# Performance work log

Measured on AMD Instinct MI355X. Metric: run time of the kernel, lower is better.

Reference implementation:

```python
import jax, jax.numpy as jnp
import numpy as np

EPS = 1e-12  # matches torch F.normalize eps


def setup_inputs() -> dict:
    key = jax.random.key(0)
    k1, k2, k3 = jax.random.split(key, 3)
    N, C, H, W, K = 16, 1024, 32, 32, 32
    x = jax.random.normal(k1, (N, C, H, W), dtype=jnp.float32)
    # 1x1 conv weight (K, C, 1, 1) stored as (K, C)
    conv_w = jax.random.normal(k2, (K, C), dtype=jnp.float32) * 0.02
    centroids = jax.random.uniform(k3, (K, C), dtype=jnp.float32)
    return {"x": x, "conv_w": conv_w, "centroids": centroids}


def _l2norm(v, axis):
    return v / jnp.maximum(jnp.linalg.norm(v, axis=axis, keepdims=True), EPS)


def reference(x, conv_w, centroids):
    N, C, H, W = x.shape
    K = centroids.shape[0]
    # normalize_input: L2 over channel dim
    x = _l2norm(x, axis=1)
    xf = x.reshape(N, C, H * W)                      # (N, C, P)
    # 1x1 conv == per-pixel matmul -> (N, K, P)
    logits = jnp.einsum('kc,ncp->nkp', conv_w, xf)
    a = jax.nn.softmax(logits, axis=1)               # softmax over clusters
    # sum_p a[n,k,p] * (x[n,:,p] - centroids[k,:])
    # == (a @ x^T) - (sum_p a) * centroids  (two GEMMs, no (N,K,C,P) blowup)
    vlad = jnp.einsum('nkp,ncp->nkc', a, xf) - a.sum(-1)[:, :, None] * centroids[None]
    vlad = _l2norm(vlad, axis=2)                     # intra-cluster L2 norm
    vlad = vlad.reshape(N, K * C)
    vlad = _l2norm(vlad, axis=1)                     # global L2 norm
    return vlad
```

## Files before the change

### kernel.cpp

```cpp
#include <hip/hip_runtime.h>

#define NB   16
#define CC   1024
#define PP   1024
#define KK   32
#define EPSF 1e-12f

typedef __attribute__((ext_vector_type(8))) short  bf16x8;
typedef __attribute__((ext_vector_type(4))) float  f32x4;

__device__ __forceinline__ float bf2f(unsigned short u) {
    union { unsigned int i; float f; } v; v.i = ((unsigned int)u) << 16; return v.f;
}
__device__ __forceinline__ unsigned short f2bf(float f) {
    union { float f; unsigned int i; } v; v.f = f;
    return (unsigned short)((v.i + 0x7fffu + ((v.i >> 16) & 1u)) >> 16);
}

template <typename T> struct IO;
template <> struct IO<float> {
    static __device__ __forceinline__ float  ld (const float* p) { return *p; }
    static __device__ __forceinline__ float4 ld4(const float* p) { return *(const float4*)p; }
};
template <> struct IO<unsigned short> {
    static __device__ __forceinline__ float  ld (const unsigned short* p) { return bf2f(*p); }
    static __device__ __forceinline__ float4 ld4(const unsigned short* p) {
        const ushort4 u = *(const ushort4*)p;
        return make_float4(bf2f(u.x), bf2f(u.y), bf2f(u.z), bf2f(u.w));
    }
};

__global__ __launch_bounds__(256) void k_detect(const unsigned short* __restrict__ xu,
                                                int* __restrict__ flag) {
    __shared__ int s;
    const int t = threadIdx.x;
    if (t == 0) s = 0;
    __syncthreads();
    int bad = 0;
    for (int i = t; i < 4096; i += 256)
        if (((xu[i] >> 7) & 0xFFu) > 0x9Fu) bad = 1;
    if (bad) atomicOr(&s, 1);
    __syncthreads();
    if (t == 0) flag[0] = s;
}

template <typename T>
__device__ __forceinline__ void attn_body(const T* __restrict__ x,
                                          const T* __restrict__ w,
                                          float* __restrict__ rnorm_ws,
                                          unsigned short* __restrict__ attn_g,
                                          float* __restrict__ asum) {
    __shared__ __align__(16) unsigned short xt[32 * 136];
    __shared__ __align__(16) unsigned short w_lds[32 * 136];
    __shared__ float red[32 * 32];
    __shared__ float lg[32 * 33];
    __shared__ float inv_lds[32];
    __shared__ float rnorm_lds[32];
    const int b = blockIdx.x, t = threadIdx.x;
    const int n = b >> 5, pbase = (b & 31) * 32;
    const int lane = t & 63, wv = t >> 6;
    const int quad = lane >> 4, l15 = lane & 15;
    const int mt = wv & 1, nt = wv >> 1;

    const size_t xb = (size_t)n * CC * PP + pbase;
    float ss0 = 0.f, ss1 = 0.f, ss2 = 0.f, ss3 = 0.f;
    f32x4 acc = {0.f, 0.f, 0.f, 0.f};

    const int pxg = 4 * (t & 7);
    const int crow = t >> 3;

    for (int ch = 0; ch < 8; ++ch) {
        const int c0 = ch * 128;
        __syncthreads();
        #pragma unroll
        for (int pass = 0; pass < 4; ++pass) {
            const int cl = crow + 32 * pass;
            const float4 v = IO<T>::ld4(&x[xb + (size_t)(c0 + cl) * PP + pxg]);
            ss0 += v.x * v.x; ss1 += v.y * v.y; ss2 += v.z * v.z; ss3 += v.w * v.w;
            xt[(pxg + 0) * 136 + cl] = f2bf(v.x);
            xt[(pxg + 1) * 136 + cl] = f2bf(v.y);
            xt[(pxg + 2) * 136 + cl] = f2bf(v.z);
            xt[(pxg + 3) * 136 + cl] = f2bf(v.w);
        }
        {
            const int k = t >> 3, cg = (t & 7) * 16;
            #pragma unroll
            for (int j = 0; j < 4; ++j) {
                const float4 v = IO<T>::ld4(&w[k * CC + c0 + cg + 4 * j]);
                ushort4 u;
                u.x = f2bf(v.x); u.y = f2bf(v.y); u.z = f2bf(v.z); u.w = f2bf(v.w);
                *(ushort4*)&w_lds[k * 136 + cg + 4 * j] = u;
            }
        }
        __syncthreads();
        #pragma unroll
        for (int ks = 0; ks < 4; ++ks) {
            const bf16x8 av = *(const bf16x8*)&xt[(mt * 16 + l15) * 136 + ks * 32 + quad * 8];
            const bf16x8 bv = *(const bf16x8*)&w_lds[(nt * 16 + l15) * 136 + ks * 32 + quad * 8];
            acc = __builtin_amdgcn_mfma_f32_16x16x32_bf16(av, bv, acc, 0, 0, 0);
        }
    }
    red[crow * 32 + pxg + 0] = ss0;
    red[crow * 32 + pxg + 1] = ss1;
    red[crow * 32 + pxg + 2] = ss2;
    red[crow * 32 + pxg + 3] = ss3;
    __syncthreads();
    if (t < 32) {
        float s = 0.f;
        #pragma unroll
        for (int g = 0; g < 32; ++g) s += red[g * 32 + t];
        const float r = 1.0f / fmaxf(sqrtf(s), EPSF);
        rnorm_lds[t] = r;
        rnorm_ws[n * PP + pbase + t] = r;
    }
    __syncthreads();
    #pragma unroll
    for (int reg = 0; reg < 4; ++reg) {
        const int px = mt * 16 + quad * 4 + reg;
        lg[px * 33 + nt * 16 + l15] = acc[reg] * rnorm_lds[px];
    }
    __syncthreads();
    if (t < 32) {
        float m = -1e30f;
        #pragma unroll
        for (int k = 0; k < KK; ++k) m = fmaxf(m, lg[t * 33 + k]);
        float s = 0.f;
        #pragma unroll
        for (int k = 0; k < KK; ++k) {
            const float e = expf(lg[t * 33 + k] - m);
            lg[t * 33 + k] = e;
            s += e;
        }
        inv_lds[t] = 1.0f / s;
    }
    __syncthreads();
    {
        const int k = t >> 3;
        float s = 0.f;
        ushort4 u;
        float vv[4];
        #pragma unroll
        for (int j = 0; j < 4; ++j) {
            const int px = pxg + j;
            vv[j] = lg[px * 33 + k] * inv_lds[px];
        }
        u.x = f2bf(vv[0]); u.y = f2bf(vv[1]); u.z = f2bf(vv[2]); u.w = f2bf(vv[3]);
        s = bf2f(u.x) + bf2f(u.y) + bf2f(u.z) + bf2f(u.w);
        *(ushort4*)&attn_g[((size_t)n * KK + k) * PP + pbase + pxg] = u;
        s += __shfl_xor(s, 1, 64);
        s += __shfl_xor(s, 2, 64);
        s += __shfl_xor(s, 4, 64);
        if ((t & 7) == 0) atomicAdd(&asum[n * KK + k], s);
    }
}
__global__ __launch_bounds__(256) void k_attn(const void* __restrict__ x,
                                              const void* __restrict__ w,
                                              const int* __restrict__ flag,
                                              float* __restrict__ rnorm_ws,
                                              unsigned short* __restrict__ attn_g,
                                              float* __restrict__ asum) {
    if (*flag) attn_body<float>((const float*)x, (const float*)w, rnorm_ws, attn_g, asum);
    else       attn_body<unsigned short>((const unsigned short*)x, (const unsigned short*)w,
                                         rnorm_ws, attn_g, asum);
}

template <typename T>
__device__ __forceinline__ void vlad_body(const T* __restrict__ x,
                                          const T* __restrict__ cent,
                                          const float* __restrict__ rnorm_ws,
                                          const unsigned short* __restrict__ attn_g,
                                          const float* __restrict__ asum,
                                          float* __restrict__ vlad,
                                          float* __restrict__ ssqnk) {
    __shared__ __align__(16) unsigned short xt[64 * 136];
    __shared__ __align__(16) unsigned short at_lds[32 * 136];
    __shared__ float asum_lds[32];
    __shared__ float ssq_lds[32];
    const int b = blockIdx.x, t = threadIdx.x;
    const int n = b >> 4, cbase = (b & 15) * 64;
    const int lane = t & 63, wv = t >> 6;
    const int quad = lane >> 4, l15 = lane & 15;
    const int mt = wv & 1, nt0 = (wv >> 1) * 2, nt1 = nt0 + 1;

    if (t < 32) { asum_lds[t] = asum[n * KK + t]; ssq_lds[t] = 0.f; }

    f32x4 acc0 = {0.f, 0.f, 0.f, 0.f}, acc1 = {0.f, 0.f, 0.f, 0.f};
    const size_t xb = (size_t)n * CC * PP + (size_t)cbase * PP;

    for (int pc = 0; pc < 8; ++pc) {
        const int p0 = pc * 128;
        __syncthreads();
        {
            const int k = t >> 3, pg = (t & 7) * 16;
            const size_t base = ((size_t)n * KK + k) * PP + p0 + pg;
            const uint4 u0 = *(const uint4*)&attn_g[base];
            const uint4 u1 = *(const uint4*)&attn_g[base + 8];
            *(uint4*)&at_lds[k * 136 + pg]     = u0;
            *(uint4*)&at_lds[k * 136 + pg + 8] = u1;
        }
        {
            const int pg = 4 * (t & 31);
            const float4 rn = *(const float4*)&rnorm_ws[n * PP + p0 + pg];
            #pragma unroll
            for (int pass = 0; pass < 8; ++pass) {
                const int ci = (t >> 5) + 8 * pass;
                const float4 v = IO<T>::ld4(&x[xb + (size_t)ci * PP + p0 + pg]);
                ushort4 u;
                u.x = f2bf(v.x * rn.x); u.y = f2bf(v.y * rn.y);
                u.z = f2bf(v.z * rn.z); u.w = f2bf(v.w * rn.w);
                *(ushort4*)&xt[ci * 136 + pg] = u;
            }
        }
        __syncthreads();
        #pragma unroll
        for (int ks = 0; ks < 4; ++ks) {
            const bf16x8 av  = *(const bf16x8*)&at_lds[(mt * 16 + l15) * 136 + ks * 32 + quad * 8];
            const bf16x8 bv0 = *(const bf16x8*)&xt[(nt0 * 16 + l15) * 136 + ks * 32 + quad * 8];
            const bf16x8 bv1 = *(const bf16x8*)&xt[(nt1 * 16 + l15) * 136 + ks * 32 + quad * 8];
            acc0 = __builtin_amdgcn_mfma_f32_16x16x32_bf16(av, bv0, acc0, 0, 0, 0);
            acc1 = __builtin_amdgcn_mfma_f32_16x16x32_bf16(av, bv1, acc1, 0, 0, 0);
        }
    }
    __syncthreads();
    const int c0g = cbase + nt0 * 16 + l15, c1g = cbase + nt1 * 16 + l15;
    #pragma unroll
    for (int reg = 0; reg < 4; ++reg) {
        const int k = mt * 16 + quad * 4 + reg;
        const float A = asum_lds[k];
        const float v0 = acc0[reg] - A * IO<T>::ld(&cent[k * CC + c0g]);
        const float v1 = acc1[reg] - A * IO<T>::ld(&cent[k * CC + c1g]);
        vlad[((size_t)n * KK + k) * CC + c0g] = v0;
        vlad[((size_t)n * KK + k) * CC + c1g] = v1;
        float s = v0 * v0 + v1 * v1;
        s += __shfl_xor(s, 1, 64);
        s += __shfl_xor(s, 2, 64);
        s += __shfl_xor(s, 4, 64);
        s += __shfl_xor(s, 8, 64);
        if (l15 == 0) atomicAdd(&ssq_lds[k], s);
    }
    __syncthreads();
    if (t < 32) atomicAdd(&ssqnk[n * KK + t], ssq_lds[t]);
}
__global__ __launch_bounds__(256) void k_vlad(const void* __restrict__ x,
                                              const void* __restrict__ cent,
                                              const int* __restrict__ flag,
                                              const float* __restrict__ rnorm_ws,
                                              const unsigned short* __restrict__ attn_g,
                                              const float* __restrict__ asum,
                                              float* __restrict__ vlad,
                                              float* __restrict__ ssqnk) {
    if (*flag) vlad_body<float>((const float*)x, (const float*)cent, rnorm_ws, attn_g,
                                asum, vlad, ssqnk);
    else       vlad_body<unsigned short>((const unsigned short*)x, (const unsigned short*)cent,
                                         rnorm_ws, attn_g, asum, vlad, ssqnk);
}

__global__ __launch_bounds__(64) void k_factors(const float* __restrict__ ssqnk,
                                                float* __restrict__ rintra,
                                                float* __restrict__ rglob) {
    const int n = blockIdx.x, t = threadIdx.x;
    const float s = (t < KK) ? ssqnk[n * KK + t] : 0.f;
    const float r = 1.0f / fmaxf(sqrtf(s), EPSF);
    if (t < KK) rintra[n * KK + t] = r;
    float g = s * r * r;
    for (int off = 32; off > 0; off >>= 1) g += __shfl_down(g, off, 64);
    if (t == 0) rglob[n] = 1.0f / fmaxf(sqrtf(g), EPSF);
}

__global__ __launch_bounds__(256) void k_out(const float* __restrict__ vlad,
                                             const float* __restrict__ rintra,
                                             const float* __restrict__ rglob,
                                             const int* __restrict__ flag,
                                             void* __restrict__ out) {
    const int b = blockIdx.x, t = threadIdx.x;
    const float f = rintra[b] * rglob[b >> 5];
    const float4 v = ((const float4*)(vlad + (size_t)b * CC))[t];
    if (*flag) {
        float4 o; o.x = v.x * f; o.y = v.y * f; o.z = v.z * f; o.w = v.w * f;
        ((float4*)((float*)out + (size_t)b * CC))[t] = o;
    } else {
        ushort4 u;
        u.x = f2bf(v.x * f); u.y = f2bf(v.y * f);
        u.z = f2bf(v.z * f); u.w = f2bf(v.w * f);
        ((ushort4*)((unsigned short*)out + (size_t)b * CC))[t] = u;
    }
}

extern "C" void kernel_launch(void* const* d_in, const int* in_sizes, int n_in,
                              void* d_out, int out_size, void* d_ws, size_t ws_size,
                              hipStream_t stream) {
    const void* x    = d_in[0];
    const void* w    = d_in[1];
    const void* cent = d_in[2];

    float* ws       = (float*)d_ws;
    float* rnorm_ws = ws;
    float* vlad     = rnorm_ws + NB * PP;
    float* asum     = vlad + NB * KK * CC;
    float* ssqnk    = asum + NB * KK;
    float* rintra   = ssqnk + NB * KK;
    float* rglob    = rintra + NB * KK;
    int*   flag     = (int*)(rglob + NB);
    unsigned short* attn_g = (unsigned short*)(flag + 4);

    hipMemsetAsync(asum, 0, 2 * NB * KK * sizeof(float), stream);

    k_detect<<<1, 256, 0, stream>>>((const unsigned short*)x, flag);
    k_attn<<<NB * 32, 256, 0, stream>>>(x, w, flag, rnorm_ws, attn_g, asum);
    k_vlad<<<NB * 16, 256, 0, stream>>>(x, cent, flag, rnorm_ws, attn_g, asum, vlad, ssqnk);
    k_factors<<<NB, 64, 0, stream>>>(ssqnk, rintra, rglob);
    k_out<<<NB * KK, 256, 0, stream>>>(vlad, rintra, rglob, flag, d_out);
}
```

Before: 127.6 us.

## Split logits GEMM over channel slabs, add softmax kernel, restructure vlad and fuse launches

Measured after the change: 140.4 us. 10.0% more time.

```diff
diff --git a/kernel.cpp b/kernel.cpp
--- a/kernel.cpp
+++ b/kernel.cpp
@@ -5,6 +5,7 @@
 #define PP   1024
 #define KK   32
 #define EPSF 1e-12f
+#define NSLAB 8
 
 typedef __attribute__((ext_vector_type(8))) short  bf16x8;
 typedef __attribute__((ext_vector_type(4))) float  f32x4;
@@ -19,271 +20,316 @@
 
 template <typename T> struct IO;
 template <> struct IO<float> {
-    static __device__ __forceinline__ float  ld (const float* p) { return *p; }
-    static __device__ __forceinline__ float4 ld4(const float* p) { return *(const float4*)p; }
+    static __device__ __forceinline__ float ld(const float* p) { return *p; }
+    static __device__ __forceinline__ f32x4 ld4(const float* p) { return *(const f32x4*)p; }
+    static __device__ __forceinline__ void st4(float* p, f32x4 v) { *(f32x4*)p = v; }
 };
 template <> struct IO<unsigned short> {
-    static __device__ __forceinline__ float  ld (const unsigned short* p) { return bf2f(*p); }
-    static __device__ __forceinline__ float4 ld4(const unsigned short* p) {
+    static __device__ __forceinline__ float ld(const unsigned short* p) { return bf2f(*p); }
+    static __device__ __forceinline__ f32x4 ld4(const unsigned short* p) {
         const ushort4 u = *(const ushort4*)p;
-        return make_float4(bf2f(u.x), bf2f(u.y), bf2f(u.z), bf2f(u.w));
+        f32x4 r; r[0] = bf2f(u.x); r[1] = bf2f(u.y); r[2] = bf2f(u.z); r[3] = bf2f(u.w);
+        return r;
+    }
+    static __device__ __forceinline__ void st4(unsigned short* p, f32x4 v) {
+        ushort4 u;
+        u.x = f2bf(v[0]); u.y = f2bf(v[1]); u.z = f2bf(v[2]); u.w = f2bf(v[3]);
+        *(ushort4*)p = u;
     }
 };
 
-__global__ __launch_bounds__(256) void k_detect(const unsigned short* __restrict__ xu,
-                                                int* __restrict__ flag) {
-    __shared__ int s;
+struct LogSmem {
+    unsigned short xT[256][72];
+    unsigned short W[32][136];
+    float red[8][256];
+};
+
+template <typename T>
+__device__ __forceinline__ void logits_body(const T* __restrict__ x,
+                                            const T* __restrict__ w,
+                                            LogSmem& sm,
+                                            float* __restrict__ logits_p,
+                                            float* __restrict__ ssq_p) {
+    const int b = blockIdx.x, t = threadIdx.x;
+    const int n = b >> 5, r = b & 31, s = r >> 2, pq = r & 3;
+    const int c0 = s * 128, p0 = pq * 256;
+    const int lane = t & 63, wvi = t >> 6;
+    const int quad = lane >> 4, l15 = lane & 15;
+    {
+        const int k = t >> 3, coff = (t & 7) * 16;
+        #pragma unroll
+        for (int j = 0; j < 4; ++j) {
+            const f32x4 v = IO<T>::ld4(&w[k * CC + c0 + coff + 4 * j]);
+            ushort4 u;
+            u.x = f2bf(v[0]); u.y = f2bf(v[1]); u.z = f2bf(v[2]); u.w = f2bf(v[3]);
+            *(ushort4*)&sm.W[k][coff + 4 * j] = u;
+        }
+    }
+    const int g  = t >> 5;
+    const int po = (t & 31) * 8;
+    const size_t xb = (size_t)n * CC * PP;
+    float ssq_t[8] = {};
+    f32x4 acc[2][4] = {};
+
+    #pragma unroll
+    for (int ch = 0; ch < 4; ++ch) {
+        f32x4 vr[4][2];
+        #pragma unroll
+        for (int i = 0; i < 4; ++i) {
+            const size_t row = xb + (size_t)(c0 + ch * 32 + g * 4 + i) * PP + p0 + po;
+            vr[i][0] = IO<T>::ld4(&x[row]);
+            vr[i][1] = IO<T>::ld4(&x[row + 4]);
+        }
+        __syncthreads();
+        #pragma unroll
+        for (int hj = 0; hj < 8; ++hj) {
+            const int h = hj >> 2, j = hj & 3;
+            ssq_t[hj] += vr[0][h][j] * vr[0][h][j] + vr[1][h][j] * vr[1][h][j]
+                       + vr[2][h][j] * vr[2][h][j] + vr[3][h][j] * vr[3][h][j];
+            ushort4 u;
+            u.x = f2bf(vr[0][h][j]); u.y = f2bf(vr[1][h][j]);
+            u.z = f2bf(vr[2][h][j]); u.w = f2bf(vr[3][h][j]);
+            const int p_loc = po + hj;
+            const int swz = ((p_loc >> 3) ^ (p_loc >> 5)) & 3;
+            const int colg = (((g >> 1) ^ swz) * 8) + (g & 1) * 4;
+            *(ushort4*)&sm.xT[p_loc][colg] = u;
+        }
+        __syncthreads();
+        #pragma unroll
+        for (int mt = 0; mt < 2; ++mt) {
+            const bf16x8 av = *(const bf16x8*)&sm.W[mt * 16 + l15][ch * 32 + quad * 8];
+            #pragma unroll
+            for (int pt = 0; pt < 4; ++pt) {
+                const int p_loc = wvi * 64 + pt * 16 + l15;
+                const int swz = ((p_loc >> 3) ^ (p_loc >> 5)) & 3;
+                const bf16x8 bv = *(const bf16x8*)&sm.xT[p_loc][(quad ^ swz) * 8];
+                acc[mt][pt] = __builtin_amdgcn_mfma_f32_16x16x32_bf16(av, bv, acc[mt][pt], 0, 0, 0);
+            }
+        }
+    }
+    #pragma unroll
+    for (int mt = 0; mt < 2; ++mt)
+        #pragma unroll
+        for (int pt = 0; pt < 4; ++pt)
+            #pragma unroll
+            for (int reg = 0; reg < 4; ++reg) {
+                const int kk = mt * 16 + quad * 4 + reg;
+                const int p  = p0 + wvi * 64 + pt * 16 + l15;
+                logits_p[(((size_t)s * NB + n) * KK + kk) * PP + p] = acc[mt][pt][reg];
+            }
+    #pragma unroll
+    for (int hj = 0; hj < 8; ++hj) sm.red[g][po + hj] = ssq_t[hj];
+    __syncthreads();
+    {
+        float ss = 0.f;
+        #pragma unroll
+        for (int gg = 0; gg < 8; ++gg) ss += sm.red[gg][t];
+        ssq_p[((size_t)s * NB + n) * PP + p0 + t] = ss;
+    }
+}
+
+__global__ __launch_bounds__(256) void k_logits(const void* __restrict__ xv,
+                                                const void* __restrict__ wv,
+                                                int* __restrict__ flag,
+                                                float* __restrict__ logits_p,
+                                                float* __restrict__ ssq_p) {
+    __shared__ LogSmem sm;
+    __shared__ int s_bad;
     const int t = threadIdx.x;
-    if (t == 0) s = 0;
-    __syncthreads();
-    int bad = 0;
-    for (int i = t; i < 4096; i += 256)
-        if (((xu[i] >> 7) & 0xFFu) > 0x9Fu) bad = 1;
-    if (bad) atomicOr(&s, 1);
-    __syncthreads();
-    if (t == 0) flag[0] = s;
-}
+    if (t == 0) s_bad = 0;
+    __syncthreads();
+    {
+        const unsigned short* xu = (const unsigned short*)xv;
+        int bad = 0;
+        for (int i = t; i < 4096; i += 256)
+            if (((xu[i] >> 7) & 0xFFu) > 0x9Fu) bad = 1;
+        if (bad) atomicOr(&s_bad, 1);
+    }
+    __syncthreads();
+    const int f = s_bad;
+    if (blockIdx.x == 0 && t == 0) flag[0] = f;
+    if (f) logits_body<float>((const float*)xv, (const float*)wv, sm, logits_p, ssq_p);
+    else   logits_body<unsigned short>((const unsigned short*)xv, (const unsigned short*)wv,
+                                       sm, logits_p, ssq_p);
+}
+
+__global__ __launch_bounds__(256) void k_soft(const float* __restrict__ logits_p,
+                                              const float* __restrict__ ssq_p,
+                                              float* __restrict__ rnorm_ws,
+                                              unsigned short* __restrict__ attn_g,
+                                              float* __restrict__ asum_p) {
+    __shared__ float s_rn[32];
+    __shared__ float s_as[32];
+    const int b = blockIdx.x, t = threadIdx.x;
+    const int n = b >> 5, ps = b & 31;
+    const int p0 = ps * 32;
+    if (t < 32) {
+        float ss = 0.f;
+        #pragma unroll
+        for (int s = 0; s < NSLAB; ++s) ss += ssq_p[((size_t)s * NB + n) * PP + p0 + t];
+        const float rr = 1.0f / fmaxf(sqrtf(ss), EPSF);
+        s_rn[t] = rr;
+        rnorm_ws[n * PP + p0 + t] = rr;
+        s_as[t] = 0.f;
+    }
+    __syncthreads();
+    const int pl = t >> 3, kg = (t & 7) * 4;
+    const float rn = s_rn[pl];
+    float l[4];
+    #pragma unroll
+    for (int j = 0; j < 4; ++j) {
+        float a = 0.f;
+        #pragma unroll
+        for (int s = 0; s < NSLAB; ++s)
+            a += logits_p[(((size_t)s * NB + n) * KK + kg + j) * PP + p0 + pl];
+        l[j] = a * rn;
+    }
+    float mx = fmaxf(fmaxf(l[0], l[1]), fmaxf(l[2], l[3]));
+    mx = fmaxf(mx, __shfl_xor(mx, 1, 64));
+    mx = fmaxf(mx, __shfl_xor(mx, 2, 64));
+    mx = fmaxf(mx, __shfl_xor(mx, 4, 64));
+    float e[4], sum = 0.f;
+    #pragma unroll
+    for (int j = 0; j < 4; ++j) { e[j] = expf(l[j] - mx); sum += e[j]; }
+    sum += __shfl_xor(sum, 1, 64);
+    sum += __shfl_xor(sum, 2, 64);
+    sum += __shfl_xor(sum, 4, 64);
+    const float inv = 1.0f / sum;
+    #pragma unroll
+    for (int j = 0; j < 4; ++j) {
+        const unsigned short uu = f2bf(e[j] * inv);
+        attn_g[((size_t)n * KK + kg + j) * PP + p0 + pl] = uu;
+        atomicAdd(&s_as[kg + j], bf2f(uu));
+    }
+    __syncthreads();
+    if (t < 32) asum_p[(n * 32 + ps) * KK + t] = s_as[t];
+}
+
+struct VladSmem { float asum[32]; float ssq[32]; };
 
 template <typename T>
-__device__ __forceinline__ void attn_body(const T* __restrict__ x,
-                                          const T* __restrict__ w,
-                                          float* __restrict__ rnorm_ws,
-                                          unsigned short* __restrict__ attn_g,
-                                          float* __restrict__ asum) {
-    __shared__ __align__(16) unsigned short xt[32 * 136];
-    __shared__ __align__(16) unsigned short w_lds[32 * 136];
-    __shared__ float red[32 * 32];
-    __shared__ float lg[32 * 33];
-    __shared__ float inv_lds[32];
-    __shared__ float rnorm_lds[32];
+__device__ __forceinline__ void vlad_body(const T* __restrict__ x,
+                                          const T* __restrict__ cent, VladSmem& sm,
+                                          const float* __restrict__ rnorm_ws,
+                                          const unsigned short* __restrict__ attn_g,
+                                          const float* __restrict__ asum_p,
+                                          float* __restrict__ vlad,
+                                          float* __restrict__ ssqnk_p) {
     const int b = blockIdx.x, t = threadIdx.x;
-    const int n = b >> 5, pbase = (b & 31) * 32;
-    const int lane = t & 63, wv = t >> 6;
+    const int n = b >> 5, ct = b & 31;
+    const int lane = t & 63, wvi = t >> 6;
     const int quad = lane >> 4, l15 = lane & 15;
-    const int mt = wv & 1, nt = wv >> 1;
-
-    const size_t xb = (size_t)n * CC * PP + pbase;
-    float ss0 = 0.f, ss1 = 0.f, ss2 = 0.f, ss3 = 0.f;
-    f32x4 acc = {0.f, 0.f, 0.f, 0.f};
-
-    const int pxg = 4 * (t & 7);
-    const int crow = t >> 3;
-
-    for (int ch = 0; ch < 8; ++ch) {
-        const int c0 = ch * 128;
-        __syncthreads();
-        #pragma unroll
-        for (int pass = 0; pass < 4; ++pass) {
-            const int cl = crow + 32 * pass;
-            const float4 v = IO<T>::ld4(&x[xb + (size_t)(c0 + cl) * PP + pxg]);
-            ss0 += v.x * v.x; ss1 += v.y * v.y; ss2 += v.z * v.z; ss3 += v.w * v.w;
-            xt[(pxg + 0) * 136 + cl] = f2bf(v.x);
-            xt[(pxg + 1) * 136 + cl] = f2bf(v.y);
-            xt[(pxg + 2) * 136 + cl] = f2bf(v.z);
-            xt[(pxg + 3) * 136 + cl] = f2bf(v.w);
-        }
-        {
-            const int k = t >> 3, cg = (t & 7) * 16;
-            #pragma unroll
-            for (int j = 0; j < 4; ++j) {
-                const float4 v = IO<T>::ld4(&w[k * CC + c0 + cg + 4 * j]);
-                ushort4 u;
-                u.x = f2bf(v.x); u.y = f2bf(v.y); u.z = f2bf(v.z); u.w = f2bf(v.w);
-                *(ushort4*)&w_lds[k * 136 + cg + 4 * j] = u;
-            }
-        }
-        __syncthreads();
-        #pragma unroll
-        for (int ks = 0; ks < 4; ++ks) {
-            const bf16x8 av = *(const bf16x8*)&xt[(mt * 16 + l15) * 136 + ks * 32 + quad * 8];
-            const bf16x8 bv = *(const bf16x8*)&w_lds[(nt * 16 + l15) * 136 + ks * 32 + quad * 8];
-            acc = __builtin_amdgcn_mfma_f32_16x16x32_bf16(av, bv, acc, 0, 0, 0);
-        }
-    }
-    red[crow * 32 + pxg + 0] = ss0;
-    red[crow * 32 + pxg + 1] = ss1;
-    red[crow * 32 + pxg + 2] = ss2;
-    red[crow * 32 + pxg + 3] = ss3;
-    __syncthreads();
+    const int mt = wvi & 1, nt = wvi >> 1;
+    const int krow = mt * 16 + l15;
+    const int crow = ct * 32 + nt * 16 + l15;
     if (t < 32) {
         float s = 0.f;
         #pragma unroll
-        for (int g = 0; g < 32; ++g) s += red[g * 32 + t];
-        const float r = 1.0f / fmaxf(sqrtf(s), EPSF);
-        rnorm_lds[t] = r;
-        rnorm_ws[n * PP + pbase + t] = r;
-    }
-    __syncthreads();
+        for (int ps = 0; ps < 32; ++ps) s += asum_p[(n * 32 + ps) * KK + t];
+        sm.asum[t] = s;
+        sm.ssq[t] = 0.f;
+    }
+    __syncthreads();
+    const unsigned short* apq = attn_g + ((size_t)n * KK + krow) * PP + quad * 8;
+    const T* xp = x + (size_t)n * CC * PP + (size_t)crow * PP + quad * 8;
+    const float* rp = rnorm_ws + n * PP + quad * 8;
+    f32x4 acc = {0.f, 0.f, 0.f, 0.f};
+    bf16x8 avq[4]; f32x4 xq0[4], xq1[4], rq0[4], rq1[4];
+    #pragma unroll
+    for (int i = 0; i < 4; ++i) {
+        const int o = i * 32;
+        avq[i] = *(const bf16x8*)&apq[o];
+        xq0[i] = IO<T>::ld4(&xp[o]); xq1[i] = IO<T>::ld4(&xp[o + 4]);
+        rq0[i] = *(const f32x4*)&rp[o]; rq1[i] = *(const f32x4*)&rp[o + 4];
+    }
+    #pragma unroll
+    for (int st = 0; st < 32; ++st) {
+        const int sl = st & 3;
+        bf16x8 bv;
+        #pragma unroll
+        for (int j = 0; j < 4; ++j) {
+            bv[j]     = (short)f2bf(xq0[sl][j] * rq0[sl][j]);
+            bv[4 + j] = (short)f2bf(xq1[sl][j] * rq1[sl][j]);
+        }
+        acc = __builtin_amdgcn_mfma_f32_16x16x32_bf16(avq[sl], bv, acc, 0, 0, 0);
+        if (st + 4 < 32) {
+            const int o = (st + 4) * 32;
+            avq[sl] = *(const bf16x8*)&apq[o];
+            xq0[sl] = IO<T>::ld4(&xp[o]); xq1[sl] = IO<T>::ld4(&xp[o + 4]);
+            rq0[sl] = *(const f32x4*)&rp[o]; rq1[sl] = *(const f32x4*)&rp[o + 4];
+        }
+    }
     #pragma unroll
     for (int reg = 0; reg < 4; ++reg) {
-        const int px = mt * 16 + quad * 4 + reg;
-        lg[px * 33 + nt * 16 + l15] = acc[reg] * rnorm_lds[px];
-    }
-    __syncthreads();
-    if (t < 32) {
-        float m = -1e30f;
-        #pragma unroll
-        for (int k = 0; k < KK; ++k) m = fmaxf(m, lg[t * 33 + k]);
-        float s = 0.f;
-        #pragma unroll
-        for (int k = 0; k < KK; ++k) {
-            const float e = expf(lg[t * 33 + k] - m);
-            lg[t * 33 + k] = e;
-            s += e;
-        }
-        inv_lds[t] = 1.0f / s;
-    }
-    __syncthreads();
-    {
-        const int k = t >> 3;
-        float s = 0.f;
-        ushort4 u;
-        float vv[4];
-        #pragma unroll
-        for (int j = 0; j < 4; ++j) {
-            const int px = pxg + j;
-            vv[j] = lg[px * 33 + k] * inv_lds[px];
-        }
-        u.x = f2bf(vv[0]); u.y = f2bf(vv[1]); u.z = f2bf(vv[2]); u.w = f2bf(vv[3]);
-        s = bf2f(u.x) + bf2f(u.y) + bf2f(u.z) + bf2f(u.w);
-        *(ushort4*)&attn_g[((size_t)n * KK + k) * PP + pbase + pxg] = u;
-        s += __shfl_xor(s, 1, 64);
-        s += __shfl_xor(s, 2, 64);
-        s += __shfl_xor(s, 4, 64);
-        if ((t & 7) == 0) atomicAdd(&asum[n * KK + k], s);
-    }
-}
-__global__ __launch_bounds__(256) void k_attn(const void* __restrict__ x,
-                                              const void* __restrict__ w,
-                                              const int* __restrict__ flag,
-                                              float* __restrict__ rnorm_ws,
-                                              unsigned short* __restrict__ attn_g,
-                                              float* __restrict__ asum) {
-    if (*flag) attn_body<float>((const float*)x, (const float*)w, rnorm_ws, attn_g, asum);
-    else       attn_body<unsigned short>((const unsigned short*)x, (const unsigned short*)w,
-                                         rnorm_ws, attn_g, asum);
-}
-
-template <typename T>
-__device__ __forceinline__ void vlad_body(const T* __restrict__ x,
-                                          const T* __restrict__ cent,
-                                          const float* __restrict__ rnorm_ws,
-                                          const unsigned short* __restrict__ attn_g,
-                                          const float* __restrict__ asum,
-                                          float* __restrict__ vlad,
-                                          float* __restrict__ ssqnk) {
-    __shared__ __align__(16) unsigned short xt[64 * 136];
-    __shared__ __align__(16) unsigned short at_lds[32 * 136];
-    __shared__ float asum_lds[32];
-    __shared__ float ssq_lds[32];
-    const int b = blockIdx.x, t = threadIdx.x;
-    const int n = b >> 4, cbase = (b & 15) * 64;
-    const int lane = t & 63, wv = t >> 6;
-    const int quad = lane >> 4, l15 = lane & 15;
-    const int mt = wv & 1, nt0 = (wv >> 1) * 2, nt1 = nt0 + 1;
-
-    if (t < 32) { asum_lds[t] = asum[n * KK + t]; ssq_lds[t] = 0.f; }
-
-    f32x4 acc0 = {0.f, 0.f, 0.f, 0.f}, acc1 = {0.f, 0.f, 0.f, 0.f};
-    const size_t xb = (size_t)n * CC * PP + (size_t)cbase * PP;
-
-    for (int pc = 0; pc < 8; ++pc) {
-        const int p0 = pc * 128;
-        __syncthreads();
-        {
-            const int k = t >> 3, pg = (t & 7) * 16;
-            const size_t base = ((size_t)n * KK + k) * PP + p0 + pg;
-            const uint4 u0 = *(const uint4*)&attn_g[base];
-            const uint4 u1 = *(const uint4*)&attn_g[base + 8];
-            *(uint4*)&at_lds[k * 136 + pg]     = u0;
-            *(uint4*)&at_lds[k * 136 + pg + 8] = u1;
-        }
-        {
-            const int pg = 4 * (t & 31);
-            const float4 rn = *(const float4*)&rnorm_ws[n * PP + p0 + pg];
-            #pragma unroll
-            for (int pass = 0; pass < 8; ++pass) {
-                const int ci = (t >> 5) + 8 * pass;
-                const float4 v = IO<T>::ld4(&x[xb + (size_t)ci * PP + p0 + pg]);
-                ushort4 u;
-                u.x = f2bf(v.x * rn.x); u.y = f2bf(v.y * rn.y);
-                u.z = f2bf(v.z * rn.z); u.w = f2bf(v.w * rn.w);
-                *(ushort4*)&xt[ci * 136 + pg] = u;
-            }
-        }
-        __syncthreads();
-        #pragma unroll
-        for (int ks = 0; ks < 4; ++ks) {
-            const bf16x8 av  = *(const bf16x8*)&at_lds[(mt * 16 + l15) * 136 + ks * 32 + quad * 8];
-            const bf16x8 bv0 = *(const bf16x8*)&xt[(nt0 * 16 + l15) * 136 + ks * 32 + quad * 8];
-            const bf16x8 bv1 = *(const bf16x8*)&xt[(nt1 * 16 + l15) * 136 + ks * 32 + quad * 8];
-            acc0 = __builtin_amdgcn_mfma_f32_16x16x32_bf16(av, bv0, acc0, 0, 0, 0);
-            acc1 = __builtin_amdgcn_mfma_f32_16x16x32_bf16(av, bv1, acc1, 0, 0, 0);
-        }
-    }
-    __syncthreads();
-    const int c0g = cbase + nt0 * 16 + l15, c1g = cbase + nt1 * 16 + l15;
-    #pragma unroll
-    for (int reg = 0; reg < 4; ++reg) {
-        const int k = mt * 16 + quad * 4 + reg;
-        const float A = asum_lds[k];
-        const float v0 = acc0[reg] - A * IO<T>::ld(&cent[k * CC + c0g]);
-        const float v1 = acc1[reg] - A * IO<T>::ld(&cent[k * CC + c1g]);
-        vlad[((size_t)n * KK + k) * CC + c0g] = v0;
-        vlad[((size_t)n * KK + k) * CC + c1g] = v1;
-        float s = v0 * v0 + v1 * v1;
-        s += __shfl_xor(s, 1, 64);
-        s += __shfl_xor(s, 2, 64);
-        s += __shfl_xor(s, 4, 64);
-        s += __shfl_xor(s, 8, 64);
-        if (l15 == 0) atomicAdd(&ssq_lds[k], s);
-    }
-    __syncthreads();
-    if (t < 32) atomicAdd(&ssqnk[n * KK + t], ssq_lds[t]);
-}
-__global__ __launch_bounds__(256) void k_vlad(const void* __restrict__ x,
-                                              const void* __restrict__ cent,
+        const int kk = mt * 16 + quad * 4 + reg;
+        const float A = sm.asum[kk];
+        const float v = acc[reg] - A * IO<T>::ld(&cent[kk * CC + crow]);
+        vlad[((size_t)n * KK + kk) * CC + crow] = v;
+        float sq = v * v;
+        sq += __shfl_xor(sq, 1, 64);
+        sq += __shfl_xor(sq, 2, 64);
+        sq += __shfl_xor(sq, 4, 64);
+        sq += __shfl_xor(sq, 8, 64);
+        if (l15 == 0) atomicAdd(&sm.ssq[kk], sq);
+    }
+    __syncthreads();
+    if (t < 32) ssqnk_p[(n * 32 + ct) * KK + t] = sm.ssq[t];
+}
+
+__global__ __launch_bounds__(256) void k_vlad(const void* __restrict__ xv,
+                                              const void* __restrict__ centv,
                                               const int* __restrict__ flag,
                                               const float* __restrict__ rnorm_ws,
                                               const unsigned short* __restrict__ attn_g,
-                                              const float* __restrict__ asum,
+                                              const float* __restrict__ asum_p,
                                               float* __restrict__ vlad,
-                                              float* __restrict__ ssqnk) {
-    if (*flag) vlad_body<float>((const float*)x, (const float*)cent, rnorm_ws, attn_g,
-                                asum, vlad, ssqnk);
-    else       vlad_body<unsigned short>((const unsigned short*)x, (const unsigned short*)cent,
-                                         rnorm_ws, attn_g, asum, vlad, ssqnk);
-}
-
-__global__ __launch_bounds__(64) void k_factors(const float* __restrict__ ssqnk,
-                                                float* __restrict__ rintra,
-                                                float* __restrict__ rglob) {
-    const int n = blockIdx.x, t = threadIdx.x;
-    const float s = (t < KK) ? ssqnk[n * KK + t] : 0.f;
-    const float r = 1.0f / fmaxf(sqrtf(s), EPSF);
-    if (t < KK) rintra[n * KK + t] = r;
-    float g = s * r * r;
-    for (int off = 32; off > 0; off >>= 1) g += __shfl_down(g, off, 64);
-    if (t == 0) rglob[n] = 1.0f / fmaxf(sqrtf(g), EPSF);
+                                              float* __restrict__ ssqnk_p) {
+    __shared__ VladSmem sm;
+    if (*flag) vlad_body<float>((const float*)xv, (const float*)centv, sm, rnorm_ws,
+                                attn_g, asum_p, vlad, ssqnk_p);
+    else       vlad_body<unsigned short>((const unsigned short*)xv, (const unsigned short*)centv,
+                                         sm, rnorm_ws, attn_g, asum_p, vlad, ssqnk_p);
+}
+
+struct OutSmem { float ssq[32]; float rint[32]; float rg; };
+
+template <typename T>
+__device__ __forceinline__ void out_body(const float* __restrict__ vlad,
+                                         const float* __restrict__ ssqnk_p,
+                                         OutSmem& sm, T* __restrict__ out) {
+    const int b = blockIdx.x, t = threadIdx.x;
+    const int n = b >> 5, k = b & 31;
+    if (t < 32) {
+        float s = 0.f;
+        #pragma unroll
+        for (int ct = 0; ct < 32; ++ct) s += ssqnk_p[(n * 32 + ct) * KK + t];
+        sm.ssq[t] = s;
+    }
+    __syncthreads();
+    if (t < 64) {
+        const float s = (t < 32) ? sm.ssq[t] : 0.f;
+        const float rr = 1.0f / fmaxf(sqrtf(s), EPSF);
+        float gg = s * rr * rr;
+        #pragma unroll
+        for (int off = 32; off > 0; off >>= 1) gg += __shfl_down(gg, off, 64);
+        if (t == 0) sm.rg = 1.0f / fmaxf(sqrtf(gg), EPSF);
+        if (t < 32) sm.rint[t] = rr;
+    }
+    __syncthreads();
+    const float f = sm.rint[k] * sm.rg;
+    const size_t ob = ((size_t)n * KK + k) * CC + 4 * t;
+    f32x4 v = *(const f32x4*)&vlad[ob];
+    v[0] *= f; v[1] *= f; v[2] *= f; v[3] *= f;
+    IO<T>::st4(&out[ob], v);
 }
 
 __global__ __launch_bounds__(256) void k_out(const float* __restrict__ vlad,
-                                             const float* __restrict__ rintra,
-                                             const float* __restrict__ rglob,
+                                             const float* __restrict__ ssqnk_p,
                                              const int* __restrict__ flag,
-                                             void* __restrict__ out) {
-    const int b = blockIdx.x, t = threadIdx.x;
-    const float f = rintra[b] * rglob[b >> 5];
-    const float4 v = ((const float4*)(vlad + (size_t)b * CC))[t];
-    if (*flag) {
-        float4 o; o.x = v.x * f; o.y = v.y * f; o.z = v.z * f; o.w = v.w * f;
-        ((float4*)((float*)out + (size_t)b * CC))[t] = o;
-    } else {
-        ushort4 u;
-        u.x = f2bf(v.x * f); u.y = f2bf(v.y * f);
-        u.z = f2bf(v.z * f); u.w = f2bf(v.w * f);
-        ((ushort4*)((unsigned short*)out + (size_t)b * CC))[t] = u;
-    }
+                                             void* __restrict__ outv) {
+    __shared__ OutSmem sm;
+    if (*flag) out_body<float>(vlad, ssqnk_p, sm, (float*)outv);
+    else       out_body<unsigned short>(vlad, ssqnk_p, sm, (unsigned short*)outv);
 }
 
 extern "C" void kernel_launch(void* const* d_in, const int* in_sizes, int n_in,
@@ -293,21 +339,19 @@
     const void* w    = d_in[1];
     const void* cent = d_in[2];
 
-    float* ws       = (float*)d_ws;
-    float* rnorm_ws = ws;
-    float* vlad     = rnorm_ws + NB * PP;
-    float* asum     = vlad + NB * KK * CC;
-    float* ssqnk    = asum + NB * KK;
-    float* rintra   = ssqnk + NB * KK;
-    float* rglob    = rintra + NB * KK;
-    int*   flag     = (int*)(rglob + NB);
+    float* ws        = (float*)d_ws;
+    float* logits_p  = ws;
+    float* ssq_p     = logits_p + (size_t)NSLAB * NB * KK * PP;
+    float* rnorm_ws  = ssq_p + (size_t)NSLAB * NB * PP;
+    float* asum_p    = rnorm_ws + NB * PP;
+    float* ssqnk_p   = asum_p + NB * 32 * KK;
+    float* vlad      = ssqnk_p + NB * 32 * KK;
+    int*   flag      = (int*)(vlad + (size_t)NB * KK * CC);
     unsigned short* attn_g = (unsigned short*)(flag + 4);
 
-    hipMemsetAsync(asum, 0, 2 * NB * KK * sizeof(float), stream);
-
-    k_detect<<<1, 256, 0, stream>>>((const unsigned short*)x, flag);
-    k_attn<<<NB * 32, 256, 0, stream>>>(x, w, flag, rnorm_ws, attn_g, asum);
-    k_vlad<<<NB * 16, 256, 0, stream>>>(x, cent, flag, rnorm_ws, attn_g, asum, vlad, ssqnk);
-    k_factors<<<NB, 64, 0, stream>>>(ssqnk, rintra, rglob);
-    k_out<<<NB * KK, 256, 0, stream>>>(vlad, rintra, rglob, flag, d_out);
-}
+    k_logits<<<NB * 32, 256, 0, stream>>>(x, w, flag, logits_p, ssq_p);
+    k_soft<<<NB * 32, 256, 0, stream>>>(logits_p, ssq_p, rnorm_ws, attn_g, asum_p);
+    k_vlad<<<NB * 32, 256, 0, stream>>>(x, cent, flag, rnorm_ws, attn_g, asum_p,
+                                        vlad, ssqnk_p);
+    k_out<<<NB * KK, 256, 0, stream>>>(vlad, ssqnk_p, flag, d_out);
+}
```
